# Kernel tuning notes

Hardware: AMD Instinct MI355X
Metric: run time of the kernel (lower is better)

Reference implementation:

```python
import jax, jax.numpy as jnp
import numpy as np

B, S, D = 2, 2048, 2048
E, K, F = 8, 2, 4096
EPS_LN = 1e-5
EPS_AUX = 1e-9


def setup_inputs() -> dict:
    key = jax.random.key(0)
    ks = jax.random.split(key, 12)
    s_d = 1.0 / np.sqrt(D)
    s_f = 1.0 / np.sqrt(F)
    return {
        "x": jax.random.normal(ks[0], (B, S, D), dtype=jnp.float32),
        # router LayerNorm
        "ln_gamma": jnp.ones((D,), jnp.float32),
        "ln_beta": jnp.zeros((D,), jnp.float32),
        # router MLP: Linear(D,D) -> ReLU -> Linear(D,E)
        "rW1": jax.random.uniform(ks[1], (D, D), jnp.float32, -s_d, s_d),
        "rb1": jnp.zeros((D,), jnp.float32),
        "rW2": jax.random.uniform(ks[2], (D, E), jnp.float32, -s_d, s_d),
        "rb2": jnp.zeros((E,), jnp.float32),
        # experts: per-expert FFN D -> F -> D
        "We1": jax.random.uniform(ks[3], (E, D, F), jnp.float32, -s_d, s_d),
        "be1": jnp.zeros((E, F), jnp.float32),
        "We2": jax.random.uniform(ks[4], (E, F, D), jnp.float32, -s_f, s_f),
        "be2": jnp.zeros((E, D), jnp.float32),
    }


def _layer_norm(x, gamma, beta):
    mu = jnp.mean(x, axis=-1, keepdims=True)
    var = jnp.mean(jnp.square(x - mu), axis=-1, keepdims=True)
    return (x - mu) * jax.lax.rsqrt(var + EPS_LN) * gamma + beta


def reference(x, ln_gamma, ln_beta, rW1, rb1, rW2, rb2, We1, be1, We2, be2):
    # --- BaseRouter ---
    x_norm = _layer_norm(x, ln_gamma, ln_beta)
    h = jax.nn.relu(jnp.einsum("bsd,de->bse", x_norm, rW1) + rb1)
    router_logits = jnp.einsum("bsd,de->bse", h, rW2) + rb2  # [B,S,E]
    router_probs = jax.nn.softmax(router_logits, axis=-1)

    top_k_probs, top_k_indices = jax.lax.top_k(router_probs, K)  # [B,S,K]
    top_k_probs = top_k_probs / jnp.sum(top_k_probs, axis=-1, keepdims=True)

    # aux load-balance loss (detached in original via .item())
    p_mean = jnp.mean(router_probs, axis=(0, 1))  # [E]
    aux_loss = jnp.sum(p_mean * jnp.log(p_mean * E + EPS_AUX))

    # --- dispatch / combine weights: scatter top-k probs to [B,S,E] ---
    one_hot = jax.nn.one_hot(top_k_indices, E, dtype=x.dtype)  # [B,S,K,E]
    combine = jnp.einsum("bske,bsk->bse", one_hot, top_k_probs)  # [B,S,E]

    # --- experts: dense per-expert FFN, weighted combine ---
    eh = jax.nn.relu(jnp.einsum("bsd,edf->ebsf", x, We1) + be1[:, None, None, :])
    ey = jnp.einsum("ebsf,efd->ebsd", eh, We2) + be2[:, None, None, :]
    out = jnp.einsum("ebsd,bse->bsd", ey, combine)

    return out, aux_loss
```

## Files before the change

kernel.cpp:

```cpp
#include <hip/hip_runtime.h>
#include <hip/hip_bf16.h>

#define NTOK 4096
#define DIM  2048
#define NEXP 8
#define FDIM 4096
#define NPAIR 8192

typedef __attribute__((ext_vector_type(4))) float     f32x4;
typedef __attribute__((ext_vector_type(8))) short     s16x8;
typedef __attribute__((ext_vector_type(4))) short     s16x4;
typedef __attribute__((ext_vector_type(8))) _Float16  f16x8;
typedef __attribute__((ext_vector_type(4))) _Float16  f16x4;

#define DEVI static __device__ __forceinline__

DEVI void gl2lds(const void* g, void* l) {
  __builtin_amdgcn_global_load_lds((const __attribute__((address_space(1))) unsigned int*)g,
                                   (__attribute__((address_space(3))) unsigned int*)l, 16, 0, 0);
}

DEVI float bf2f(unsigned short s) {
  unsigned int u = ((unsigned int)s) << 16; float f; __builtin_memcpy(&f, &u, 4); return f;
}
DEVI unsigned short f2bf(float f) {
  __hip_bfloat16 h = __float2bfloat16(f); unsigned short s; __builtin_memcpy(&s, &h, 2); return s;
}
DEVI float wredsum(float v) {
#pragma unroll
  for (int o = 32; o > 0; o >>= 1) v += __shfl_xor(v, o);
  return v;
}

__global__ __launch_bounds__(256) void ln_conv_kernel(
    const float* __restrict__ x, const float* __restrict__ gamma, const float* __restrict__ beta,
    _Float16* __restrict__ xh, _Float16* __restrict__ xl, unsigned short* __restrict__ xbf)
{
  int tok = blockIdx.x;
  int tid = threadIdx.x, lane = tid & 63, wv = tid >> 6;
  const float* xr = x + (size_t)tok * DIM;
  float v[8];
  *(float4*)(v)     = *(const float4*)(xr + tid * 8);
  *(float4*)(v + 4) = *(const float4*)(xr + tid * 8 + 4);
  float s = v[0]+v[1]+v[2]+v[3]+v[4]+v[5]+v[6]+v[7];
  __shared__ float red[4];
  s = wredsum(s);
  if (lane == 0) red[wv] = s;
  __syncthreads();
  float mu = (red[0]+red[1]+red[2]+red[3]) * (1.f / DIM);
  __syncthreads();
  float s2 = 0.f;
#pragma unroll
  for (int j = 0; j < 8; j++) { float d = v[j] - mu; s2 += d * d; }
  s2 = wredsum(s2);
  if (lane == 0) red[wv] = s2;
  __syncthreads();
  float var = (red[0]+red[1]+red[2]+red[3]) * (1.f / DIM);
  float rs = 1.0f / sqrtf(var + 1e-5f);

  float4 g0 = *(const float4*)(gamma + tid*8), g1 = *(const float4*)(gamma + tid*8 + 4);
  float4 b0 = *(const float4*)(beta  + tid*8), b1 = *(const float4*)(beta  + tid*8 + 4);
  float gg[8] = {g0.x,g0.y,g0.z,g0.w,g1.x,g1.y,g1.z,g1.w};
  float bb[8] = {b0.x,b0.y,b0.z,b0.w,b1.x,b1.y,b1.z,b1.w};
  f16x8 vh, vl; s16x8 vb;
#pragma unroll
  for (int j = 0; j < 8; j++) {
    float xn = (v[j] - mu) * rs * gg[j] + bb[j];
    _Float16 h = (_Float16)xn;
    vh[j] = h;
    vl[j] = (_Float16)((xn - (float)h) * 4096.f);
    vb[j] = (short)f2bf(v[j]);
  }
  *(f16x8*)(xh + (size_t)tok*DIM + tid*8) = vh;
  *(f16x8*)(xl + (size_t)tok*DIM + tid*8) = vl;
  *(s16x8*)(xbf + (size_t)tok*DIM + tid*8) = vb;
}

__global__ __launch_bounds__(256) void transpose_bf16_kernel(
    const float* __restrict__ src, unsigned short* __restrict__ dst, int R, int C)
{
  src += (size_t)blockIdx.z * R * C;
  dst += (size_t)blockIdx.z * R * C;
  __shared__ float tile[64][65];
  int r0 = blockIdx.y * 64, c0 = blockIdx.x * 64;
  int tx = threadIdx.x & 15, ty = threadIdx.x >> 4;
#pragma unroll
  for (int i = 0; i < 4; i++) {
    float4 v = *(const float4*)(src + (size_t)(r0 + ty*4 + i) * C + c0 + tx*4);
    tile[ty*4+i][tx*4+0] = v.x; tile[ty*4+i][tx*4+1] = v.y;
    tile[ty*4+i][tx*4+2] = v.z; tile[ty*4+i][tx*4+3] = v.w;
  }
  __syncthreads();
#pragma unroll
  for (int i = 0; i < 4; i++) {
    int c = c0 + ty*4 + i;
    s16x4 o;
    o[0] = (short)f2bf(tile[tx*4+0][ty*4+i]); o[1] = (short)f2bf(tile[tx*4+1][ty*4+i]);
    o[2] = (short)f2bf(tile[tx*4+2][ty*4+i]); o[3] = (short)f2bf(tile[tx*4+3][ty*4+i]);
    *(s16x4*)(dst + (size_t)c * R + r0 + tx*4) = o;
  }
}

__global__ __launch_bounds__(256) void transpose_f16split_kernel(
    const float* __restrict__ src, _Float16* __restrict__ dh, _Float16* __restrict__ dl, int R, int C)
{
  __shared__ float tile[64][65];
  int r0 = blockIdx.y * 64, c0 = blockIdx.x * 64;
  int tx = threadIdx.x & 15, ty = threadIdx.x >> 4;
#pragma unroll
  for (int i = 0; i < 4; i++) {
    float4 v = *(const float4*)(src + (size_t)(r0 + ty*4 + i) * C + c0 + tx*4);
    tile[ty*4+i][tx*4+0] = v.x; tile[ty*4+i][tx*4+1] = v.y;
    tile[ty*4+i][tx*4+2] = v.z; tile[ty*4+i][tx*4+3] = v.w;
  }
  __syncthreads();
#pragma unroll
  for (int i = 0; i < 4; i++) {
    int c = c0 + ty*4 + i;
    f16x4 oh, ol;
#pragma unroll
    for (int j = 0; j < 4; j++) {
      float f = tile[tx*4+j][ty*4+i];
      _Float16 h = (_Float16)f;
      oh[j] = h;
      ol[j] = (_Float16)((f - (float)h) * 4096.f);
    }
    *(f16x4*)(dh + (size_t)c * R + r0 + tx*4) = oh;
    *(f16x4*)(dl + (size_t)c * R + r0 + tx*4) = ol;
  }
}

#define R_TA 10240
#define R_TB 5120
__global__ __launch_bounds__(256) void router_gemm_kernel(
    const _Float16* __restrict__ Ah, const _Float16* __restrict__ Al,
    const _Float16* __restrict__ Bh, const _Float16* __restrict__ Bl,
    const float* __restrict__ bias, float* __restrict__ Cout)
{
  __shared__ char lds[2*R_TA + 2*R_TB];
  char* lAh = lds;             char* lAl = lds + R_TA;
  char* lBh = lds + 2*R_TA;    char* lBl = lds + 2*R_TA + R_TB;
  const int K = DIM;
  int m0 = blockIdx.y * 128, n0 = blockIdx.x * 64;
  int tid = threadIdx.x, lane = tid & 63, wv = tid >> 6;
  int wm = wv >> 1, wn = wv & 1;

  const char* srcAh[3]; const char* srcAl[3];
  const char* srcBh[2]; const char* srcBl[2];
  {
    int i = 0;
    for (int c = wv; c < 10; c += 4, i++) {
      int doff = c*1024 + lane*16;
      int row = doff / 80; int b = doff - row*80; if (b >= 64) b = 0;
      srcAh[i] = (const char*)(Ah + (size_t)(m0+row)*K) + b;
      srcAl[i] = (const char*)(Al + (size_t)(m0+row)*K) + b;
    }
    i = 0;
    for (int c = wv; c < 5; c += 4, i++) {
      int doff = c*1024 + lane*16;
      int row = doff / 80; int b = doff - row*80; if (b >= 64) b = 0;
      srcBh[i] = (const char*)(Bh + (size_t)(n0+row)*K) + b;
      srcBl[i] = (const char*)(Bl + (size_t)(n0+row)*K) + b;
    }
  }

  f32x4 acc1[4][2], acc2[4][2];
#pragma unroll
  for (int mb = 0; mb < 4; mb++)
#pragma unroll
    for (int nb = 0; nb < 2; nb++) {
      acc1[mb][nb] = (f32x4){0.f,0.f,0.f,0.f};
      acc2[mb][nb] = (f32x4){0.f,0.f,0.f,0.f};
    }

  for (int kt = 0; kt < K/32; kt++) {
    {
      int i = 0;
      for (int c = wv; c < 10; c += 4, i++) {
        gl2lds(srcAh[i], lAh + c*1024);
        gl2lds(srcAl[i], lAl + c*1024);
        srcAh[i] += 64; srcAl[i] += 64;
      }
      i = 0;
      for (int c = wv; c < 5; c += 4, i++) {
        gl2lds(srcBh[i], lBh + c*1024);
        gl2lds(srcBl[i], lBl + c*1024);
        srcBh[i] += 64; srcBl[i] += 64;
      }
    }
    __syncthreads();
    int kb = (lane >> 4) * 16;
    f16x8 ah[4], al[4], bh[2], bl[2];
#pragma unroll
    for (int mb = 0; mb < 4; mb++) {
      int r = wm*64 + mb*16 + (lane & 15);
      ah[mb] = *(const f16x8*)(lAh + r*80 + kb);
      al[mb] = *(const f16x8*)(lAl + r*80 + kb);
    }
#pragma unroll
    for (int nb = 0; nb < 2; nb++) {
      int r = wn*32 + nb*16 + (lane & 15);
      bh[nb] = *(const f16x8*)(lBh + r*80 + kb);
      bl[nb] = *(const f16x8*)(lBl + r*80 + kb);
    }
#pragma unroll
    for (int mb = 0; mb < 4; mb++)
#pragma unroll
      for (int nb = 0; nb < 2; nb++) {
        acc1[mb][nb] = __builtin_amdgcn_mfma_f32_16x16x32_f16(ah[mb], bh[nb], acc1[mb][nb], 0,0,0);
        acc2[mb][nb] = __builtin_amdgcn_mfma_f32_16x16x32_f16(ah[mb], bl[nb], acc2[mb][nb], 0,0,0);
        acc2[mb][nb] = __builtin_amdgcn_mfma_f32_16x16x32_f16(al[mb], bh[nb], acc2[mb][nb], 0,0,0);
      }
    __syncthreads();
  }
#pragma unroll
  for (int mb = 0; mb < 4; mb++)
#pragma unroll
    for (int nb = 0; nb < 2; nb++) {
      int col = n0 + wn*32 + nb*16 + (lane & 15);
      float bv = bias[col];
#pragma unroll
      for (int r = 0; r < 4; r++) {
        int m = m0 + wm*64 + mb*16 + (lane >> 4)*4 + r;
        float hval = acc1[mb][nb][r] + acc2[mb][nb][r] * (1.f/4096.f) + bv;
        Cout[(size_t)m*DIM + col] = fmaxf(hval, 0.f);
      }
    }
}

__global__ __launch_bounds__(256) void router_logits_kernel(
    const float* __restrict__ h, const float* __restrict__ rW2, const float* __restrict__ rb2,
    float* __restrict__ probs,
    int* __restrict__ eid, float* __restrict__ wts)
{
  int lane = threadIdx.x & 63, wv = threadIdx.x >> 6;
  int tok = blockIdx.x * 4 + wv;
  const float* hr = h + (size_t)tok * DIM;
  float lg[8] = {0,0,0,0,0,0,0,0};
#pragma unroll
  for (int j = 0; j < 8; j++) {
    int k = j * 256 + lane * 4;
    float4 hv = *(const float4*)(hr + k);
    float hv4[4] = {hv.x, hv.y, hv.z, hv.w};
#pragma unroll
    for (int r = 0; r < 4; r++) {
      const float4* w4 = (const float4*)(rW2 + (size_t)(k + r) * NEXP);
      float4 wa = w4[0], wb = w4[1];
      lg[0] += hv4[r]*wa.x; lg[1] += hv4[r]*wa.y; lg[2] += hv4[r]*wa.z; lg[3] += hv4[r]*wa.w;
      lg[4] += hv4[r]*wb.x; lg[5] += hv4[r]*wb.y; lg[6] += hv4[r]*wb.z; lg[7] += hv4[r]*wb.w;
    }
  }
#pragma unroll
  for (int e = 0; e < 8; e++) {
#pragma unroll
    for (int o = 32; o > 0; o >>= 1) lg[e] += __shfl_xor(lg[e], o);
  }
  if (lane == 0) {
    float l[8], p[8];
    float m = -1e30f;
#pragma unroll
    for (int e = 0; e < 8; e++) { l[e] = lg[e] + rb2[e]; m = fmaxf(m, l[e]); }
    float s = 0.f;
#pragma unroll
    for (int e = 0; e < 8; e++) { p[e] = expf(l[e] - m); s += p[e]; }
    float inv = 1.f / s;
#pragma unroll
    for (int e = 0; e < 8; e++) { p[e] *= inv; probs[(size_t)tok*8 + e] = p[e]; }
    int i0 = 0;
#pragma unroll
    for (int e = 1; e < 8; e++) if (p[e] > p[i0]) i0 = e;
    int i1 = (i0 == 0) ? 1 : 0;
#pragma unroll
    for (int e = 0; e < 8; e++) if (e != i0 && p[e] > p[i1]) i1 = e;
    float denom = 1.f / (p[i0] + p[i1]);
    eid[tok*2+0] = i0; eid[tok*2+1] = i1;
    wts[tok*2+0] = p[i0]*denom; wts[tok*2+1] = p[i1]*denom;
  }
}

__global__ __launch_bounds__(256) void router_sort_kernel(
    const int* __restrict__ eid, const float* __restrict__ probs,
    int* __restrict__ cnt, int* __restrict__ basep,
    int* __restrict__ tokenlist, int* __restrict__ pairslot,
    float* __restrict__ aux_out)
{
  __shared__ int hist[256][8];
  __shared__ float wsum[4][8];
  __shared__ int bl[8];
  __shared__ int lcnt[8];
  int t = threadIdx.x, lane = t & 63, wv = t >> 6;

  int me[32];
  {
    const int4* ep = (const int4*)(eid + t * 32);
#pragma unroll
    for (int q = 0; q < 8; q++) {
      int4 v = ep[q];
      me[q*4+0] = v.x; me[q*4+1] = v.y; me[q*4+2] = v.z; me[q*4+3] = v.w;
    }
  }
#pragma unroll
  for (int e = 0; e < 8; e++) {
    int ce = 0;
#pragma unroll
    for (int i = 0; i < 32; i++) ce += (me[i] == e) ? 1 : 0;
    hist[t][e] = ce;
  }

  float part[8] = {0,0,0,0,0,0,0,0};
  for (int i = 0; i < 16; i++) {
    const float4* p4 = (const float4*)(probs + (size_t)(t*16 + i) * 8);
    float4 a = p4[0], b = p4[1];
    part[0]+=a.x; part[1]+=a.y; part[2]+=a.z; part[3]+=a.w;
    part[4]+=b.x; part[5]+=b.y; part[6]+=b.z; part[7]+=b.w;
  }
#pragma unroll
  for (int e = 0; e < 8; e++) {
#pragma unroll
    for (int o = 32; o > 0; o >>= 1) part[e] += __shfl_xor(part[e], o);
  }
  if (lane == 0) {
#pragma unroll
    for (int e = 0; e < 8; e++) wsum[wv][e] = part[e];
  }
  __syncthreads();

  if (t < 8) {
    int running = 0;
    for (int i = 0; i < 256; i++) { int tmp = hist[i][t]; hist[i][t] = running; running += tmp; }
    lcnt[t] = running;
  }
  __syncthreads();
  if (t == 0) {
    int b = 0; float aux = 0.f;
#pragma unroll
    for (int e = 0; e < 8; e++) {
      int ce = lcnt[e];
      bl[e] = b; basep[e] = b; cnt[e] = ce; b += ce;
      float pm = (wsum[0][e]+wsum[1][e]+wsum[2][e]+wsum[3][e]) * (1.f / NTOK);
      aux += pm * logf(pm * 8.f + 1e-9f);
    }
    *aux_out = aux;
  }
  __syncthreads();

#pragma unroll
  for (int i = 0; i < 32; i++) {
    int e = me[i];
    int r = 0;
#pragma unroll
    for (int j = 0; j < i; j++) r += (me[j] == e) ? 1 : 0;
    int slot = bl[e] + hist[t][e] + r;
    int pair = t*32 + i;
    tokenlist[slot] = pair >> 1;
    pairslot[pair] = slot;
  }
}

template<int MODE>
__global__ __launch_bounds__(256, 2) void expert_gemm_v6(
    const unsigned short* __restrict__ Abase,
    const unsigned short* __restrict__ Bbase,
    const float* __restrict__ bias,
    unsigned short* __restrict__ Cout,
    const int* __restrict__ cnt, const int* __restrict__ basep,
    const int* __restrict__ tokenlist)
{
  const int K = (MODE == 1) ? DIM : FDIM;
  const int N = (MODE == 1) ? FDIM : DIM;
  const int NTN = N / 128;
  __shared__ char lds[65536];

  int b = blockIdx.x;
  int low3 = b & 7, t2 = b >> 3;
  int mt = t2 & 31, pHi = t2 >> 5;
  int p = pHi * 8 + low3;
  int e = p / NTN, nt = p % NTN;
  int ne = cnt[e];
  if (mt * 128 >= ne) return;
  int mbase = basep[e] + mt * 128;
  int n0 = nt * 128;

  int tid = threadIdx.x, lane = tid & 63, wv = tid >> 6;
  int wm = wv >> 1, wn = wv & 1;

  const char* srcA[4]; const char* srcB[4];
  int sb = (((lane & 7) ^ ((lane >> 3) & 7)) << 4);
#pragma unroll
  for (int i = 0; i < 4; i++) {
    int c = wv + i*4;
    int row = c*8 + (lane >> 3);
    int slot = mbase + row; if (slot > NPAIR - 1) slot = NPAIR - 1;
    size_t arow = (MODE == 1) ? (size_t)tokenlist[slot] : (size_t)slot;
    srcA[i] = (const char*)(Abase + arow * K) + sb;
    srcB[i] = (const char*)(Bbase + ((size_t)e * N + n0 + row) * K) + sb;
  }

  f32x4 acc[4][4];
#pragma unroll
  for (int mb = 0; mb < 4; mb++)
#pragma unroll
    for (int nb = 0; nb < 4; nb++) acc[mb][nb] = (f32x4){0.f,0.f,0.f,0.f};

#pragma unroll
  for (int i = 0; i < 4; i++) {
    gl2lds(srcA[i], lds + (wv + i*4)*1024);
    gl2lds(srcB[i], lds + 16384 + (wv + i*4)*1024);
  }
  asm volatile("s_waitcnt vmcnt(0)\n\ts_barrier" ::: "memory");

  const int NT = K / 64;
  int rsw = (lane & 7) << 4;
  int cur = 0;
  for (int kt = 0; kt < NT; kt++) {
    char* cA = lds + cur*32768;
    char* cB = cA + 16384;
    if (kt + 1 < NT) {
      char* nA = lds + (cur^1)*32768;
      char* nB = nA + 16384;
      size_t ko = (size_t)(kt + 1) * 128;
#pragma unroll
      for (int i = 0; i < 4; i++) {
        gl2lds(srcA[i] + ko, nA + (wv + i*4)*1024);
        gl2lds(srcB[i] + ko, nB + (wv + i*4)*1024);
      }
    }
#pragma unroll
    for (int ks = 0; ks < 2; ks++) {
      int kb = (ks*64 + (lane >> 4)*16) ^ rsw;
      s16x8 af[4], bf[4];
#pragma unroll
      for (int mb = 0; mb < 4; mb++)
        af[mb] = *(const s16x8*)(cA + (wm*64 + mb*16 + (lane & 15))*128 + kb);
#pragma unroll
      for (int nb = 0; nb < 4; nb++)
        bf[nb] = *(const s16x8*)(cB + (wn*64 + nb*16 + (lane & 15))*128 + kb);
#pragma unroll
      for (int mb = 0; mb < 4; mb++)
#pragma unroll
        for (int nb = 0; nb < 4; nb++)
          acc[mb][nb] = __builtin_amdgcn_mfma_f32_16x16x32_bf16(af[mb], bf[nb], acc[mb][nb], 0,0,0);
    }
    __builtin_amdgcn_sched_barrier(0);
    asm volatile("s_waitcnt lgkmcnt(0)\n\ts_waitcnt vmcnt(0)\n\ts_barrier" ::: "memory");
    __builtin_amdgcn_sched_barrier(0);
    cur ^= 1;
  }

#pragma unroll
  for (int mb = 0; mb < 4; mb++)
#pragma unroll
    for (int nb = 0; nb < 4; nb++) {
      int col = n0 + wn*64 + nb*16 + (lane & 15);
      float bv = bias[(size_t)e * N + col];
#pragma unroll
      for (int r = 0; r < 4; r++) {
        int mloc = mt*128 + wm*64 + mb*16 + (lane >> 4)*4 + r;
        if (mloc < ne) {
          float v = acc[mb][nb][r] + bv;
          if (MODE == 1) v = fmaxf(v, 0.f);
          Cout[((size_t)basep[e] + mloc) * N + col] = f2bf(v);
        }
      }
    }
}

__global__ __launch_bounds__(256) void combine_kernel(
    const unsigned short* __restrict__ Yg, const int* __restrict__ pairslot,
    const float* __restrict__ wts, float* __restrict__ out)
{
  int tok = blockIdx.x, tid = threadIdx.x;
  int s0 = pairslot[tok*2], s1 = pairslot[tok*2+1];
  float w0 = wts[tok*2], w1 = wts[tok*2+1];
  s16x8 a = *(const s16x8*)(Yg + (size_t)s0 * DIM + tid*8);
  s16x8 b = *(const s16x8*)(Yg + (size_t)s1 * DIM + tid*8);
  float o[8];
#pragma unroll
  for (int j = 0; j < 8; j++)
    o[j] = w0 * bf2f((unsigned short)a[j]) + w1 * bf2f((unsigned short)b[j]);
  float* op = out + (size_t)tok * DIM + tid*8;
  float4 o0; o0.x=o[0]; o0.y=o[1]; o0.z=o[2]; o0.w=o[3];
  float4 o1; o1.x=o[4]; o1.y=o[5]; o1.z=o[6]; o1.w=o[7];
  *(float4*)op = o0;
  *(float4*)(op + 4) = o1;
}

extern "C" void kernel_launch(void* const* d_in, const int* in_sizes, int n_in,
                              void* d_out, int out_size, void* d_ws, size_t ws_size,
                              hipStream_t stream)
{
  (void)in_sizes; (void)n_in; (void)out_size; (void)ws_size;
  const float* x    = (const float*)d_in[0];
  const float* ln_g = (const float*)d_in[1];
  const float* ln_b = (const float*)d_in[2];
  const float* rW1  = (const float*)d_in[3];
  const float* rb1  = (const float*)d_in[4];
  const float* rW2  = (const float*)d_in[5];
  const float* rb2  = (const float*)d_in[6];
  const float* We1  = (const float*)d_in[7];
  const float* be1  = (const float*)d_in[8];
  const float* We2  = (const float*)d_in[9];
  const float* be2  = (const float*)d_in[10];
  float* out = (float*)d_out;
  float* aux_out = out + (size_t)NTOK * DIM;

  char* ws = (char*)d_ws;
  size_t off = 0;
  auto alloc = [&](size_t bytes) { char* p = ws + off; off += (bytes + 255) & ~(size_t)255; return p; };

  _Float16* XH   = (_Float16*)alloc((size_t)NTOK * DIM * 2);
  _Float16* XL   = (_Float16*)alloc((size_t)NTOK * DIM * 2);
  unsigned short* XBF = (unsigned short*)alloc((size_t)NTOK * DIM * 2);
  _Float16* RW1H = (_Float16*)alloc((size_t)DIM * DIM * 2);
  _Float16* RW1L = (_Float16*)alloc((size_t)DIM * DIM * 2);
  unsigned short* WET = (unsigned short*)alloc((size_t)NEXP * FDIM * DIM * 2);
  unsigned short* EH  = (unsigned short*)alloc((size_t)(NPAIR + 128) * FDIM * 2);
  char* HY = alloc((size_t)(NPAIR + 128) * DIM * 2 > (size_t)NTOK*DIM*4
                     ? (size_t)(NPAIR + 128) * DIM * 2 : (size_t)NTOK*DIM*4);
  float* H = (float*)HY;
  unsigned short* YG = (unsigned short*)HY;
  float* PROB = (float*)alloc((size_t)NTOK * 8 * 4);
  int* CNT  = (int*)alloc(256);
  int* BASE = CNT + 16;
  int* EID  = (int*)alloc((size_t)NPAIR * 4);
  float* WTS = (float*)alloc((size_t)NPAIR * 4);
  int* PAIRSLOT = (int*)alloc((size_t)NPAIR * 4);
  int* TOKLIST  = (int*)alloc((size_t)(NPAIR + 128) * 4);

  ln_conv_kernel<<<NTOK, 256, 0, stream>>>(x, ln_g, ln_b, XH, XL, XBF);
  transpose_f16split_kernel<<<dim3(DIM/64, DIM/64), 256, 0, stream>>>(rW1, RW1H, RW1L, DIM, DIM);
  transpose_bf16_kernel<<<dim3(FDIM/64, DIM/64, NEXP), 256, 0, stream>>>(We1, WET, DIM, FDIM);
  router_gemm_kernel<<<dim3(DIM/64, NTOK/128), 256, 0, stream>>>(XH, XL, RW1H, RW1L, rb1, H);
  router_logits_kernel<<<NTOK/4, 256, 0, stream>>>(H, rW2, rb2, PROB, EID, WTS);
  router_sort_kernel<<<1, 256, 0, stream>>>(EID, PROB, CNT, BASE, TOKLIST, PAIRSLOT, aux_out);
  expert_gemm_v6<1><<<8192, 256, 0, stream>>>(XBF, WET, be1, EH, CNT, BASE, TOKLIST);
  transpose_bf16_kernel<<<dim3(DIM/64, FDIM/64, NEXP), 256, 0, stream>>>(We2, WET, FDIM, DIM);
  expert_gemm_v6<2><<<4096, 256, 0, stream>>>(EH, WET, be2, YG, CNT, BASE, TOKLIST);
  combine_kernel<<<NTOK, 256, 0, stream>>>(YG, PAIRSLOT, WTS, out);
}
```

Baseline: 849.6 us.

## Pre-pack expert weights into MFMA fragment order and load B directly to registers

```diff
diff --git a/kernel.cpp b/kernel.cpp
--- a/kernel.cpp
+++ b/kernel.cpp
@@ -76,28 +76,38 @@
   *(s16x8*)(xbf + (size_t)tok*DIM + tid*8) = vb;
 }
 
-__global__ __launch_bounds__(256) void transpose_bf16_kernel(
+__global__ __launch_bounds__(256) void pack_b_kernel(
     const float* __restrict__ src, unsigned short* __restrict__ dst, int R, int C)
 {
-  src += (size_t)blockIdx.z * R * C;
-  dst += (size_t)blockIdx.z * R * C;
+  int e = blockIdx.z;
+  src += (size_t)e * R * C;
+  const int NTN = C >> 7, KT = R >> 6;
   __shared__ float tile[64][65];
-  int r0 = blockIdx.y * 64, c0 = blockIdx.x * 64;
+  int k0 = blockIdx.y * 64, c0 = blockIdx.x * 64;
   int tx = threadIdx.x & 15, ty = threadIdx.x >> 4;
 #pragma unroll
   for (int i = 0; i < 4; i++) {
-    float4 v = *(const float4*)(src + (size_t)(r0 + ty*4 + i) * C + c0 + tx*4);
+    float4 v = *(const float4*)(src + (size_t)(k0 + ty*4 + i) * C + c0 + tx*4);
     tile[ty*4+i][tx*4+0] = v.x; tile[ty*4+i][tx*4+1] = v.y;
     tile[ty*4+i][tx*4+2] = v.z; tile[ty*4+i][tx*4+3] = v.w;
   }
   __syncthreads();
-#pragma unroll
-  for (int i = 0; i < 4; i++) {
-    int c = c0 + ty*4 + i;
-    s16x4 o;
-    o[0] = (short)f2bf(tile[tx*4+0][ty*4+i]); o[1] = (short)f2bf(tile[tx*4+1][ty*4+i]);
-    o[2] = (short)f2bf(tile[tx*4+2][ty*4+i]); o[3] = (short)f2bf(tile[tx*4+3][ty*4+i]);
-    *(s16x4*)(dst + (size_t)c * R + r0 + tx*4) = o;
+  int nt = c0 >> 7;
+  int cnb = (c0 >> 4) & 7;
+  int kt = blockIdx.y;
+  int lane = threadIdx.x & 63, cl = threadIdx.x >> 6;
+  size_t pbase = (size_t)((e * NTN + nt) * KT + kt) * 8192;
+#pragma unroll
+  for (int i = 0; i < 2; i++) {
+    int cidx = cl + i*4;
+    int ks = cidx >> 2, cnL = cidx & 3;
+    int n_local = (cnb + cnL)*16 - cnb*16 + (lane & 15);
+    int k_local = ks*32 + (lane >> 4)*8;
+    s16x8 o;
+#pragma unroll
+    for (int j = 0; j < 8; j++) o[j] = (short)f2bf(tile[k_local + j][cnL*16 + (lane & 15)]);
+    (void)n_local;
+    *(s16x8*)(dst + pbase + (size_t)(ks*8 + cnb + cnL)*512 + lane*8) = o;
   }
 }
 
@@ -358,9 +368,9 @@
 }
 
 template<int MODE>
-__global__ __launch_bounds__(256, 2) void expert_gemm_v6(
+__global__ __launch_bounds__(256) void expert_gemm_v7(
     const unsigned short* __restrict__ Abase,
-    const unsigned short* __restrict__ Bbase,
+    const unsigned short* __restrict__ Bpack,
     const float* __restrict__ bias,
     unsigned short* __restrict__ Cout,
     const int* __restrict__ cnt, const int* __restrict__ basep,
@@ -369,7 +379,8 @@
   const int K = (MODE == 1) ? DIM : FDIM;
   const int N = (MODE == 1) ? FDIM : DIM;
   const int NTN = N / 128;
-  __shared__ char lds[65536];
+  const int KT = K / 64;
+  __shared__ char lds[32768];
 
   int b = blockIdx.x;
   int low3 = b & 7, t2 = b >> 3;
@@ -384,7 +395,7 @@
   int tid = threadIdx.x, lane = tid & 63, wv = tid >> 6;
   int wm = wv >> 1, wn = wv & 1;
 
-  const char* srcA[4]; const char* srcB[4];
+  const char* srcA[4];
   int sb = (((lane & 7) ^ ((lane >> 3) & 7)) << 4);
 #pragma unroll
   for (int i = 0; i < 4; i++) {
@@ -393,8 +404,9 @@
     int slot = mbase + row; if (slot > NPAIR - 1) slot = NPAIR - 1;
     size_t arow = (MODE == 1) ? (size_t)tokenlist[slot] : (size_t)slot;
     srcA[i] = (const char*)(Abase + arow * K) + sb;
-    srcB[i] = (const char*)(Bbase + ((size_t)e * N + n0 + row) * K) + sb;
-  }
+  }
+
+  const unsigned short* pb = Bpack + (size_t)p * KT * 8192 + (size_t)(wn * 4) * 512 + lane * 8;
 
   f32x4 acc[4][4];
 #pragma unroll
@@ -403,43 +415,38 @@
     for (int nb = 0; nb < 4; nb++) acc[mb][nb] = (f32x4){0.f,0.f,0.f,0.f};
 
 #pragma unroll
-  for (int i = 0; i < 4; i++) {
-    gl2lds(srcA[i], lds + (wv + i*4)*1024);
-    gl2lds(srcB[i], lds + 16384 + (wv + i*4)*1024);
-  }
+  for (int i = 0; i < 4; i++) gl2lds(srcA[i], lds + (wv + i*4)*1024);
   asm volatile("s_waitcnt vmcnt(0)\n\ts_barrier" ::: "memory");
 
-  const int NT = K / 64;
   int rsw = (lane & 7) << 4;
   int cur = 0;
-  for (int kt = 0; kt < NT; kt++) {
-    char* cA = lds + cur*32768;
-    char* cB = cA + 16384;
-    if (kt + 1 < NT) {
-      char* nA = lds + (cur^1)*32768;
-      char* nB = nA + 16384;
+  for (int kt = 0; kt < KT; kt++) {
+    char* cA = lds + cur*16384;
+    if (kt + 1 < KT) {
+      char* nA = lds + (cur^1)*16384;
       size_t ko = (size_t)(kt + 1) * 128;
 #pragma unroll
-      for (int i = 0; i < 4; i++) {
-        gl2lds(srcA[i] + ko, nA + (wv + i*4)*1024);
-        gl2lds(srcB[i] + ko, nB + (wv + i*4)*1024);
-      }
-    }
+      for (int i = 0; i < 4; i++) gl2lds(srcA[i] + ko, nA + (wv + i*4)*1024);
+    }
+    const unsigned short* pk = pb + (size_t)kt * 8192;
+    s16x8 bfr[2][4];
+#pragma unroll
+    for (int ks = 0; ks < 2; ks++)
+#pragma unroll
+      for (int nb = 0; nb < 4; nb++)
+        bfr[ks][nb] = *(const s16x8*)(pk + ks*4096 + nb*512);
 #pragma unroll
     for (int ks = 0; ks < 2; ks++) {
       int kb = (ks*64 + (lane >> 4)*16) ^ rsw;
-      s16x8 af[4], bf[4];
+      s16x8 af[4];
 #pragma unroll
       for (int mb = 0; mb < 4; mb++)
         af[mb] = *(const s16x8*)(cA + (wm*64 + mb*16 + (lane & 15))*128 + kb);
 #pragma unroll
-      for (int nb = 0; nb < 4; nb++)
-        bf[nb] = *(const s16x8*)(cB + (wn*64 + nb*16 + (lane & 15))*128 + kb);
-#pragma unroll
       for (int mb = 0; mb < 4; mb++)
 #pragma unroll
         for (int nb = 0; nb < 4; nb++)
-          acc[mb][nb] = __builtin_amdgcn_mfma_f32_16x16x32_bf16(af[mb], bf[nb], acc[mb][nb], 0,0,0);
+          acc[mb][nb] = __builtin_amdgcn_mfma_f32_16x16x32_bf16(af[mb], bfr[ks][nb], acc[mb][nb], 0,0,0);
     }
     __builtin_amdgcn_sched_barrier(0);
     asm volatile("s_waitcnt lgkmcnt(0)\n\ts_waitcnt vmcnt(0)\n\ts_barrier" ::: "memory");
@@ -529,12 +536,12 @@
 
   ln_conv_kernel<<<NTOK, 256, 0, stream>>>(x, ln_g, ln_b, XH, XL, XBF);
   transpose_f16split_kernel<<<dim3(DIM/64, DIM/64), 256, 0, stream>>>(rW1, RW1H, RW1L, DIM, DIM);
-  transpose_bf16_kernel<<<dim3(FDIM/64, DIM/64, NEXP), 256, 0, stream>>>(We1, WET, DIM, FDIM);
+  pack_b_kernel<<<dim3(FDIM/64, DIM/64, NEXP), 256, 0, stream>>>(We1, WET, DIM, FDIM);
   router_gemm_kernel<<<dim3(DIM/64, NTOK/128), 256, 0, stream>>>(XH, XL, RW1H, RW1L, rb1, H);
   router_logits_kernel<<<NTOK/4, 256, 0, stream>>>(H, rW2, rb2, PROB, EID, WTS);
   router_sort_kernel<<<1, 256, 0, stream>>>(EID, PROB, CNT, BASE, TOKLIST, PAIRSLOT, aux_out);
-  expert_gemm_v6<1><<<8192, 256, 0, stream>>>(XBF, WET, be1, EH, CNT, BASE, TOKLIST);
-  transpose_bf16_kernel<<<dim3(DIM/64, FDIM/64, NEXP), 256, 0, stream>>>(We2, WET, FDIM, DIM);
-  expert_gemm_v6<2><<<4096, 256, 0, stream>>>(EH, WET, be2, YG, CNT, BASE, TOKLIST);
+  expert_gemm_v7<1><<<8192, 256, 0, stream>>>(XBF, WET, be1, EH, CNT, BASE, TOKLIST);
+  pack_b_kernel<<<dim3(DIM/64, FDIM/64, NEXP), 256, 0, stream>>>(We2, WET, FDIM, DIM);
+  expert_gemm_v7<2><<<4096, 256, 0, stream>>>(EH, WET, be2, YG, CNT, BASE, TOKLIST);
   combine_kernel<<<NTOK, 256, 0, stream>>>(YG, PAIRSLOT, WTS, out);
 }
```

New measurement: 997.3 us. +17.4%, slower.
